# Optimization experiments

Measured on AMD Instinct MI355X. Metric: run time of the kernel, lower is better.

Reference implementation:

```python
import jax, jax.numpy as jnp
import numpy as np

INPUT_SIZE = 695 + 2 * 406 + 84  # 1591
HIDDEN = 1024
NUM_LAYERS = 2
B, T = 8, 2048


def _make_linear(key, fan_in, fan_out, forget_bias):
    kw, kb = jax.random.split(key)
    bound = 1.0 / np.sqrt(fan_in)
    W = jax.random.uniform(kw, (fan_in, fan_out), minval=-bound, maxval=bound, dtype=jnp.float32)
    b = jax.random.uniform(kb, (fan_out,), minval=-bound, maxval=bound, dtype=jnp.float32)
    H = fan_out // 3
    b = b.at[H:2 * H].set(forget_bias)  # init_input_passthrough: forget-gate bias = 6.0
    return W, b


def setup_inputs() -> dict:
    key = jax.random.key(0)
    k1, k2, k3, k4, k5 = jax.random.split(key, 5)
    prev_actions = jax.random.uniform(k1, (B, T, 695), dtype=jnp.float32)
    states = jax.random.uniform(k2, (B, T, 812), dtype=jnp.float32)
    metadata = jax.random.uniform(k3, (B, T, 84), dtype=jnp.float32)
    W1, b1 = _make_linear(k4, INPUT_SIZE, 3 * HIDDEN, 6.0)
    W2, b2 = _make_linear(k5, HIDDEN, 3 * HIDDEN, 6.0)
    return {"prev_actions": prev_actions, "states": states, "metadata": metadata,
            "W1": W1, "b1": b1, "W2": W2, "b2": b2}


def forget_mult(f, z):
    # c_t = f_t * z_t + (1 - f_t) * c_{t-1}, c_0 = 0; parallel (log-depth) scan over time.
    a = 1.0 - f          # decay
    b = f * z            # input term
    def combine(c1, c2):
        a1, b1 = c1
        a2, b2 = c2
        return a1 * a2, a2 * b1 + b2
    _, c = jax.lax.associative_scan(combine, (a, b), axis=-2)
    return c


def qrnn_layer(x, W, b):
    y = jnp.einsum('btd,dh->bth', x, W) + b          # [B,T,3H]
    Z, Fg, O = jnp.split(y, 3, axis=-1)
    C = forget_mult(jax.nn.sigmoid(Fg), jax.nn.relu(Z))  # [B,T,H]
    out = jax.nn.sigmoid(O) * C
    return out, C[..., -1, :]


def reference(prev_actions, states, metadata, W1, b1, W2, b2):
    x = jnp.concatenate([prev_actions, states, metadata], axis=-1)  # [B,T,1591]
    hs = []
    for W, b in ((W1, b1), (W2, b2)):
        x, h_last = qrnn_layer(x, W, b)
        hs.append(h_last)
    h = jnp.stack(hs, axis=-2)  # [B, num_layers, H]
    return x, h
```

## Files before the change

### kernel.cpp

```cpp
#include <hip/hip_runtime.h>

typedef unsigned short u16;
typedef unsigned int   u32;
typedef __attribute__((ext_vector_type(8))) short bf16x8;
typedef __attribute__((ext_vector_type(4))) float f32x4;
typedef __attribute__((ext_vector_type(2))) unsigned int u32x2;

#define B_ 8
#define T_ 2048
#define M_ 16384
#define N_ 3072
#define H_ 1024
#define L_ 64
#define NC_ 32

__device__ __forceinline__ u16 f2bf(float f) {
    union { float f; unsigned u; } v; v.f = f;
    unsigned r = v.u + 0x7FFFu + ((v.u >> 16) & 1u);
    return (u16)(r >> 16);
}
__device__ __forceinline__ float bf2f(u16 s) {
    union { unsigned u; float f; } v; v.u = ((unsigned)s) << 16;
    return v.f;
}
__device__ __forceinline__ float sigm(float x) {
    return 1.f / (1.f + __expf(-x));
}

__device__ __forceinline__ void gload_lds16(const void* g, void* l) {
    __builtin_amdgcn_global_load_lds(
        (const __attribute__((address_space(1))) unsigned int*)g,
        (__attribute__((address_space(3))) unsigned int*)l,
        16, 0, 0);
}

__global__ void concat_cast(const float* __restrict__ pa, const float* __restrict__ st,
                            const float* __restrict__ md, u16* __restrict__ x) {
    const int m = blockIdx.x;
    const float* pam = pa + (size_t)m * 695;
    const float* stm = st + (size_t)m * 812;
    const float* mdm = md + (size_t)m * 84;
    u16* xm = x + (size_t)m * 1600;
    for (int d = threadIdx.x; d < 1600; d += 256) {
        float v;
        if (d < 695)       v = pam[d];
        else if (d < 1507) v = stm[d - 695];
        else if (d < 1591) v = mdm[d - 1507];
        else               v = 0.f;
        xm[d] = f2bf(v);
    }
}

__global__ void wtrans(const float* __restrict__ W, u16* __restrict__ Wt, int K, int Kp) {
    __shared__ float tile[32][33];
    const int n0 = blockIdx.x << 5;
    const int k0 = blockIdx.y << 5;
    const int tx = threadIdx.x & 31, ty = threadIdx.x >> 5;
    #pragma unroll
    for (int i = 0; i < 32; i += 8) {
        int k = k0 + ty + i;
        tile[ty + i][tx] = (k < K) ? W[(size_t)k * N_ + n0 + tx] : 0.f;
    }
    __syncthreads();
    #pragma unroll
    for (int i = 0; i < 32; i += 8) {
        int n = n0 + ty + i;
        Wt[(size_t)n * Kp + k0 + tx] = f2bf(tile[tx][ty + i]);
    }
}

__global__ __launch_bounds__(512, 1)
void gemm8p(const u16* __restrict__ A, const u16* __restrict__ Bt,
            const float* __restrict__ bias, u16* __restrict__ Y,
            int Kp, int NK, int NBN) {
    __shared__ u16 lds[65536];
    const int tid = threadIdx.x;
    const int w = tid >> 6, l = tid & 63;
    const int wm = w >> 2, wn = w & 3;

    const int cpx = gridDim.x >> 3;
    const int xg = (blockIdx.x & 7) * cpx + (blockIdx.x >> 3);
    const int bm = xg / NBN, bn = xg % NBN;
    const int brow = bm << 8, bcol = bn << 8;

    const int srow = (w << 5) + (l >> 2);
    const int gslot = (l & 3) ^ ((l >> 3) & 3);
    const u16* ga = A  + (size_t)(brow + srow) * Kp + gslot * 8;
    const u16* gb = Bt + (size_t)(bcol + srow) * Kp + gslot * 8;
    const int ldst = w << 10;

    const int fl = ((l & 15) << 5) + ((((l >> 4) ^ ((l >> 1) & 3)) & 3) << 3);
    const int abase = wm << 12;
    const int bbase = 8192 + (wn << 11);

#define STG_A(r, kt) do {                                                      \
    gload_lds16(ga + (size_t)(kt) * 32,                   &lds[((r) << 14) + ldst]);        \
    gload_lds16(ga + (size_t)(kt) * 32 + 16 * (size_t)Kp, &lds[((r) << 14) + ldst + 512]);  \
} while (0)
#define STG_B(r, kt) do {                                                      \
    gload_lds16(gb + (size_t)(kt) * 32,                   &lds[((r) << 14) + 8192 + ldst]);       \
    gload_lds16(gb + (size_t)(kt) * 32 + 16 * (size_t)Kp, &lds[((r) << 14) + 8192 + ldst + 512]); \
} while (0)

    f32x4 acc[8][4] = {};
    bf16x8 bfr[4];

    STG_A(0, 0); STG_B(0, 0);
    STG_A(1, 1); STG_B(1, 1);
    STG_A(2, 2); STG_B(2, 2);
    asm volatile("s_waitcnt vmcnt(8)" ::: "memory");
    __builtin_amdgcn_s_barrier();
    asm volatile("" ::: "memory");

#define PH(CIH, LOADB, STAGECODE, WAITCODE) do {                               \
    bf16x8 af[4];                                                              \
    const int cb = cur << 14;                                                  \
    _Pragma("unroll")                                                          \
    for (int mi = 0; mi < 4; ++mi)                                             \
        af[mi] = *reinterpret_cast<const bf16x8*>(                             \
            &lds[cb + abase + (((CIH) * 4 + mi) << 9) + fl]);                  \
    if (LOADB) {                                                               \
        _Pragma("unroll")                                                      \
        for (int ni = 0; ni < 4; ++ni)                                         \
            bfr[ni] = *reinterpret_cast<const bf16x8*>(                        \
                &lds[cb + bbase + (ni << 9) + fl]);                            \
    }                                                                          \
    STAGECODE;                                                                 \
    WAITCODE;                                                                  \
    __builtin_amdgcn_s_barrier();                                              \
    __builtin_amdgcn_sched_barrier(0);                                         \
    __builtin_amdgcn_s_setprio(1);                                             \
    _Pragma("unroll")                                                          \
    for (int mi = 0; mi < 4; ++mi)                                             \
        _Pragma("unroll")                                                      \
        for (int ni = 0; ni < 4; ++ni)                                         \
            acc[(CIH) * 4 + mi][ni] = __builtin_amdgcn_mfma_f32_16x16x32_bf16( \
                bfr[ni], af[mi], acc[(CIH) * 4 + mi][ni], 0, 0, 0);            \
    __builtin_amdgcn_s_setprio(0);                                             \
    __builtin_amdgcn_sched_barrier(0);                                         \
} while (0)

    for (int kt = 0; kt < NK; ++kt) {
        const int cur = kt & 3;
        const int nxt = (kt + 3 < NK) ? kt + 3 : kt;
        const int nb = (kt + 3) & 3;
        PH(0, 1, { STG_A(nb, nxt); },
                 { asm volatile("s_waitcnt lgkmcnt(0)" ::: "memory"); });
        PH(1, 0, { STG_B(nb, nxt); },
                 { asm volatile("s_waitcnt vmcnt(8) lgkmcnt(0)" ::: "memory"); });
    }

    asm volatile("s_waitcnt vmcnt(0)" ::: "memory");
    __builtin_amdgcn_s_barrier();

    const int nloc0 = (wn << 6) + ((l >> 4) << 2);
    float4 bv4[4];
    #pragma unroll
    for (int nf = 0; nf < 4; ++nf)
        bv4[nf] = *reinterpret_cast<const float4*>(&bias[bcol + nloc0 + nf * 16]);
    #pragma unroll
    for (int ci = 0; ci < 8; ++ci) {
        const int mrow = (wm << 7) + ((ci >> 2) << 6) + ((ci & 3) << 4) + (l & 15);
        #pragma unroll
        for (int nf = 0; nf < 4; ++nf) {
            const int nloc = nloc0 + nf * 16;
            u32x2 p;
            p.x = (u32)f2bf(acc[ci][nf][0] + bv4[nf].x) |
                  ((u32)f2bf(acc[ci][nf][1] + bv4[nf].y) << 16);
            p.y = (u32)f2bf(acc[ci][nf][2] + bv4[nf].z) |
                  ((u32)f2bf(acc[ci][nf][3] + bv4[nf].w) << 16);
            const int off = (mrow << 8) + (((nloc >> 3) ^ (mrow & 7)) << 3) +
                            ((nloc >> 2) & 1) * 4;
            *reinterpret_cast<u32x2*>(&lds[off]) = p;
        }
    }
    asm volatile("s_waitcnt lgkmcnt(0)" ::: "memory");
    __builtin_amdgcn_s_barrier();

    #pragma unroll
    for (int rp = 0; rp < 16; ++rp) {
        const int row = (w << 5) + (rp << 1) + (l >> 5);
        const int c16 = l & 31;
        const bf16x8 v = *reinterpret_cast<const bf16x8*>(
            &lds[(row << 8) + ((c16 ^ (row & 7)) << 3)]);
        *reinterpret_cast<bf16x8*>(&Y[(size_t)(brow + row) * N_ + bcol + c16 * 8]) = v;
    }
#undef PH
#undef STG_A
#undef STG_B
}

__global__ void scan_p1(const u16* __restrict__ y, float* __restrict__ aprod,
                        float* __restrict__ cend) {
    const int hb = blockIdx.x & 1;
    const int chunk = (blockIdx.x >> 1) & (NC_ - 1);
    const int b = blockIdx.x >> 6;
    const int h = (hb << 9) + (threadIdx.x << 1);
    const u16* yb = y + ((size_t)b * T_ + (size_t)chunk * L_) * N_;
    float a0 = 1.f, a1 = 1.f, c0 = 0.f, c1 = 0.f;
    #pragma unroll 4
    for (int t = 0; t < L_; ++t) {
        const u32 zz = *reinterpret_cast<const u32*>(&yb[t * N_ + h]);
        const u32 ff = *reinterpret_cast<const u32*>(&yb[t * N_ + H_ + h]);
        const float f0 = sigm(bf2f((u16)ff));
        const float f1 = sigm(bf2f((u16)(ff >> 16)));
        const float z0 = fmaxf(bf2f((u16)zz), 0.f);
        const float z1 = fmaxf(bf2f((u16)(zz >> 16)), 0.f);
        c0 = f0 * z0 + (1.f - f0) * c0;  a0 *= (1.f - f0);
        c1 = f1 * z1 + (1.f - f1) * c1;  a1 *= (1.f - f1);
    }
    const size_t idx = ((size_t)b * NC_ + chunk) * H_ + h;
    *reinterpret_cast<float2*>(&aprod[idx]) = make_float2(a0, a1);
    *reinterpret_cast<float2*>(&cend[idx])  = make_float2(c0, c1);
}

__global__ void scan_p2(const float* __restrict__ aprod, const float* __restrict__ cend,
                        float* __restrict__ cin, float* __restrict__ hout, int layer) {
    const int b = blockIdx.x >> 2;
    const int h = ((blockIdx.x & 3) << 8) + threadIdx.x;
    float c = 0.f;
    #pragma unroll
    for (int k = 0; k < NC_; ++k) {
        const size_t idx = ((size_t)b * NC_ + k) * H_ + h;
        cin[idx] = c;
        c = aprod[idx] * c + cend[idx];
    }
    hout[(size_t)(((b << 1) + layer) << 10) + h] = c;
}

__global__ void scan_p3(const u16* __restrict__ y, const float* __restrict__ cin,
                        void* __restrict__ xout, int layer) {
    const int hb = blockIdx.x & 1;
    const int chunk = (blockIdx.x >> 1) & (NC_ - 1);
    const int b = blockIdx.x >> 6;
    const int h = (hb << 9) + (threadIdx.x << 1);
    const u16* yb = y + ((size_t)b * T_ + (size_t)chunk * L_) * N_;
    const size_t cidx = ((size_t)b * NC_ + chunk) * H_ + h;
    const float2 cv = *reinterpret_cast<const float2*>(&cin[cidx]);
    float c0 = cv.x, c1 = cv.y;
    u32*    xo_bf = (u32*)xout;
    float2* xo_f  = (float2*)xout;
    const size_t obase = ((size_t)b * T_ + (size_t)chunk * L_) * H_ + h;
    #pragma unroll 4
    for (int t = 0; t < L_; ++t) {
        const u32 zz = *reinterpret_cast<const u32*>(&yb[t * N_ + h]);
        const u32 ff = *reinterpret_cast<const u32*>(&yb[t * N_ + H_ + h]);
        const u32 oo = *reinterpret_cast<const u32*>(&yb[t * N_ + 2 * H_ + h]);
        const float f0 = sigm(bf2f((u16)ff));
        const float f1 = sigm(bf2f((u16)(ff >> 16)));
        const float z0 = fmaxf(bf2f((u16)zz), 0.f);
        const float z1 = fmaxf(bf2f((u16)(zz >> 16)), 0.f);
        c0 = f0 * z0 + (1.f - f0) * c0;
        c1 = f1 * z1 + (1.f - f1) * c1;
        const float o0 = sigm(bf2f((u16)oo)) * c0;
        const float o1 = sigm(bf2f((u16)(oo >> 16))) * c1;
        const size_t oi = obase + (size_t)t * H_;
        if (layer) xo_f[oi >> 1] = make_float2(o0, o1);
        else       xo_bf[oi >> 1] = (u32)f2bf(o0) | ((u32)f2bf(o1) << 16);
    }
}

extern "C" void kernel_launch(void* const* d_in, const int* in_sizes, int n_in,
                              void* d_out, int out_size, void* d_ws, size_t ws_size,
                              hipStream_t stream) {
    const float* pa = (const float*)d_in[0];
    const float* st = (const float*)d_in[1];
    const float* md = (const float*)d_in[2];
    const float* W1 = (const float*)d_in[3];
    const float* b1 = (const float*)d_in[4];
    const float* W2 = (const float*)d_in[5];
    const float* b2 = (const float*)d_in[6];
    float* out = (float*)d_out;

    char* ws = (char*)d_ws;
    const size_t y_bytes = (size_t)M_ * N_ * 2;
    const size_t x_bytes = (size_t)M_ * 1600 * 2;
    u16* y  = (u16*)ws;
    u16* x  = (u16*)(ws + y_bytes);
    u16* Wt = (u16*)(ws + y_bytes + x_bytes);
    char* scr = ws + y_bytes + (size_t)M_ * H_ * 2;
    const size_t sarr = (size_t)B_ * NC_ * H_ * 4;
    float* aprod = (float*)scr;
    float* cend  = (float*)(scr + sarr);
    float* cin   = (float*)(scr + 2 * sarr);

    float* hout = out + (size_t)M_ * H_;

    const int grid_g = (M_ / 256) * (N_ / 256);

    concat_cast<<<M_, 256, 0, stream>>>(pa, st, md, x);
    wtrans<<<dim3(N_ / 32, 50), 256, 0, stream>>>(W1, Wt, 1591, 1600);
    gemm8p<<<grid_g, 512, 0, stream>>>(x, Wt, b1, y, 1600, 50, N_ / 256);
    scan_p1<<<B_ * NC_ * 2, 256, 0, stream>>>(y, aprod, cend);
    scan_p2<<<32, 256, 0, stream>>>(aprod, cend, cin, hout, 0);
    scan_p3<<<B_ * NC_ * 2, 256, 0, stream>>>(y, cin, x, 0);

    wtrans<<<dim3(N_ / 32, 32), 256, 0, stream>>>(W2, Wt, 1024, 1024);
    gemm8p<<<grid_g, 512, 0, stream>>>(x, Wt, b2, y, 1024, 32, N_ / 256);
    scan_p1<<<B_ * NC_ * 2, 256, 0, stream>>>(y, aprod, cend);
    scan_p2<<<32, 256, 0, stream>>>(aprod, cend, cin, hout, 1);
    scan_p3<<<B_ * NC_ * 2, 256, 0, stream>>>(y, cin, out, 1);
}
```

Baseline: 431.7 us.

## Restructure GEMM main loop to K=64 double-buffered tiles with quadrant phases

The bf16 GEMM main loop changes from a 4-deep ring of K=32 tiles to two 64 KB buffers holding K=64 tiles. Each K step is split into four phases over output quadrants, and each phase stages one half-tile of A or B for the next step. Wave-to-fragment mapping and the LDS swizzle change to 8-slot XOR rows, and the epilogue index math is updated to match. Each barrier now covers more MFMA work, but prefetch depth drops to one tile, an extra barrier is added per phase, and the K-iteration count is halved at the call sites.

```diff
diff --git a/kernel.cpp b/kernel.cpp
--- a/kernel.cpp
+++ b/kernel.cpp
@@ -83,92 +83,111 @@
     const int bm = xg / NBN, bn = xg % NBN;
     const int brow = bm << 8, bcol = bn << 8;
 
-    const int srow = (w << 5) + (l >> 2);
-    const int gslot = (l & 3) ^ ((l >> 3) & 3);
-    const u16* ga = A  + (size_t)(brow + srow) * Kp + gslot * 8;
-    const u16* gb = Bt + (size_t)(bcol + srow) * Kp + gslot * 8;
-    const int ldst = w << 10;
-
-    const int fl = ((l & 15) << 5) + ((((l >> 4) ^ ((l >> 1) & 3)) & 3) << 3);
-    const int abase = wm << 12;
-    const int bbase = 8192 + (wn << 11);
-
-#define STG_A(r, kt) do {                                                      \
-    gload_lds16(ga + (size_t)(kt) * 32,                   &lds[((r) << 14) + ldst]);        \
-    gload_lds16(ga + (size_t)(kt) * 32 + 16 * (size_t)Kp, &lds[((r) << 14) + ldst + 512]);  \
+    const int gslot8 = (((l & 7) ^ ((l >> 3) & 7)) & 7) << 3;
+    const int srow = (w << 3) + (l >> 3);
+    const u16* pA = A  + (size_t)(brow + srow) * Kp + gslot8;
+    const u16* pB = Bt + (size_t)(bcol + srow) * Kp + gslot8;
+    const int wst = w << 9;
+
+    const int kslot0 = ((((l >> 4) ^ l) & 7) << 3);
+    const int aoff_l = ((wm << 4) + (l & 15)) * 64 + kslot0;
+    const int boff_l = ((wn << 4) + (l & 15)) * 64 + kslot0;
+
+#define STG_A(d, h, kt) do {                                                        \
+    gload_lds16(pA + (size_t)((h) * 128) * Kp + (size_t)(kt) * 64,                  \
+                &lds[(d) * 32768 + (h) * 8192 + wst]);                              \
+    gload_lds16(pA + (size_t)((h) * 128 + 64) * Kp + (size_t)(kt) * 64,             \
+                &lds[(d) * 32768 + (h) * 8192 + wst + 4096]);                       \
 } while (0)
-#define STG_B(r, kt) do {                                                      \
-    gload_lds16(gb + (size_t)(kt) * 32,                   &lds[((r) << 14) + 8192 + ldst]);       \
-    gload_lds16(gb + (size_t)(kt) * 32 + 16 * (size_t)Kp, &lds[((r) << 14) + 8192 + ldst + 512]); \
+#define STG_B(d, h, kt) do {                                                        \
+    gload_lds16(pB + (size_t)((h) * 128) * Kp + (size_t)(kt) * 64,                  \
+                &lds[(d) * 32768 + 16384 + (h) * 8192 + wst]);                      \
+    gload_lds16(pB + (size_t)((h) * 128 + 64) * Kp + (size_t)(kt) * 64,             \
+                &lds[(d) * 32768 + 16384 + (h) * 8192 + wst + 4096]);               \
 } while (0)
 
     f32x4 acc[8][4] = {};
-    bf16x8 bfr[4];
-
-    STG_A(0, 0); STG_B(0, 0);
-    STG_A(1, 1); STG_B(1, 1);
-    STG_A(2, 2); STG_B(2, 2);
-    asm volatile("s_waitcnt vmcnt(8)" ::: "memory");
+    bf16x8 afr[4][2], bfr[4][2];
+
+    STG_A(0, 0, 0); STG_B(0, 0, 0); STG_B(0, 1, 0); STG_A(0, 1, 0);
+    asm volatile("s_waitcnt vmcnt(4)" ::: "memory");
     __builtin_amdgcn_s_barrier();
     asm volatile("" ::: "memory");
 
-#define PH(CIH, LOADB, STAGECODE, WAITCODE) do {                               \
-    bf16x8 af[4];                                                              \
-    const int cb = cur << 14;                                                  \
-    _Pragma("unroll")                                                          \
-    for (int mi = 0; mi < 4; ++mi)                                             \
-        af[mi] = *reinterpret_cast<const bf16x8*>(                             \
-            &lds[cb + abase + (((CIH) * 4 + mi) << 9) + fl]);                  \
-    if (LOADB) {                                                               \
+#define PH(MH, NH, RDA, RDB, STAGECODE, LGK8) do {                             \
+    const int cb = cur << 15;                                                  \
+    if (RDA) {                                                                 \
+        const int ab = cb + (MH) * 8192 + aoff_l;                              \
         _Pragma("unroll")                                                      \
-        for (int ni = 0; ni < 4; ++ni)                                         \
-            bfr[ni] = *reinterpret_cast<const bf16x8*>(                        \
-                &lds[cb + bbase + (ni << 9) + fl]);                            \
+        for (int j = 0; j < 4; ++j) {                                          \
+            afr[j][0] = *reinterpret_cast<const bf16x8*>(&lds[ab + j * 2048]); \
+            afr[j][1] = *reinterpret_cast<const bf16x8*>(                      \
+                &lds[(ab + j * 2048) ^ 32]);                                   \
+        }                                                                      \
+    }                                                                          \
+    if (RDB) {                                                                 \
+        const int bb = cb + 16384 + (NH) * 8192 + boff_l;                      \
+        _Pragma("unroll")                                                      \
+        for (int j = 0; j < 2; ++j) {                                          \
+            bfr[(NH) * 2 + j][0] = *reinterpret_cast<const bf16x8*>(           \
+                &lds[bb + j * 4096]);                                          \
+            bfr[(NH) * 2 + j][1] = *reinterpret_cast<const bf16x8*>(           \
+                &lds[(bb + j * 4096) ^ 32]);                                   \
+        }                                                                      \
     }                                                                          \
     STAGECODE;                                                                 \
-    WAITCODE;                                                                  \
+    if (LGK8) asm volatile("s_waitcnt lgkmcnt(8)" ::: "memory");               \
+    asm volatile("s_waitcnt vmcnt(4)" ::: "memory");                           \
     __builtin_amdgcn_s_barrier();                                              \
+    asm volatile("s_waitcnt lgkmcnt(0)" ::: "memory");                         \
     __builtin_amdgcn_sched_barrier(0);                                         \
     __builtin_amdgcn_s_setprio(1);                                             \
     _Pragma("unroll")                                                          \
-    for (int mi = 0; mi < 4; ++mi)                                             \
+    for (int j = 0; j < 4; ++j)                                                \
         _Pragma("unroll")                                                      \
-        for (int ni = 0; ni < 4; ++ni)                                         \
-            acc[(CIH) * 4 + mi][ni] = __builtin_amdgcn_mfma_f32_16x16x32_bf16( \
-                bfr[ni], af[mi], acc[(CIH) * 4 + mi][ni], 0, 0, 0);            \
+        for (int j2 = 0; j2 < 2; ++j2)                                         \
+            _Pragma("unroll")                                                  \
+            for (int kk = 0; kk < 2; ++kk)                                     \
+                acc[(MH) * 4 + j][(NH) * 2 + j2] =                             \
+                    __builtin_amdgcn_mfma_f32_16x16x32_bf16(                   \
+                        bfr[(NH) * 2 + j2][kk], afr[j][kk],                    \
+                        acc[(MH) * 4 + j][(NH) * 2 + j2], 0, 0, 0);            \
     __builtin_amdgcn_s_setprio(0);                                             \
     __builtin_amdgcn_sched_barrier(0);                                         \
+    __builtin_amdgcn_s_barrier();                                              \
+    asm volatile("" ::: "memory");                                             \
 } while (0)
 
     for (int kt = 0; kt < NK; ++kt) {
-        const int cur = kt & 3;
-        const int nxt = (kt + 3 < NK) ? kt + 3 : kt;
-        const int nb = (kt + 3) & 3;
-        PH(0, 1, { STG_A(nb, nxt); },
-                 { asm volatile("s_waitcnt lgkmcnt(0)" ::: "memory"); });
-        PH(1, 0, { STG_B(nb, nxt); },
-                 { asm volatile("s_waitcnt vmcnt(8) lgkmcnt(0)" ::: "memory"); });
+        const int cur = kt & 1;
+        const int nb = cur ^ 1;
+        const int nxt = (kt + 1 < NK) ? kt + 1 : kt;
+        PH(0, 0, 1, 1, { STG_A(nb, 0, nxt); }, 1);
+        PH(0, 1, 0, 1, { STG_B(nb, 0, nxt); }, 0);
+        PH(1, 1, 1, 0, { STG_B(nb, 1, nxt); }, 0);
+        PH(1, 0, 0, 0, { STG_A(nb, 1, nxt); }, 0);
     }
 
     asm volatile("s_waitcnt vmcnt(0)" ::: "memory");
     __builtin_amdgcn_s_barrier();
 
-    const int nloc0 = (wn << 6) + ((l >> 4) << 2);
+    const int nq = (l >> 4) << 2;
     float4 bv4[4];
     #pragma unroll
     for (int nf = 0; nf < 4; ++nf)
-        bv4[nf] = *reinterpret_cast<const float4*>(&bias[bcol + nloc0 + nf * 16]);
-    #pragma unroll
-    for (int ci = 0; ci < 8; ++ci) {
-        const int mrow = (wm << 7) + ((ci >> 2) << 6) + ((ci & 3) << 4) + (l & 15);
+        bv4[nf] = *reinterpret_cast<const float4*>(
+            &bias[bcol + nf * 64 + (wn << 4) + nq]);
+    #pragma unroll
+    for (int mf = 0; mf < 8; ++mf) {
+        const int mrow = mf * 32 + (wm << 4) + (l & 15);
         #pragma unroll
         for (int nf = 0; nf < 4; ++nf) {
-            const int nloc = nloc0 + nf * 16;
+            const int nloc = nf * 64 + (wn << 4) + nq;
             u32x2 p;
-            p.x = (u32)f2bf(acc[ci][nf][0] + bv4[nf].x) |
-                  ((u32)f2bf(acc[ci][nf][1] + bv4[nf].y) << 16);
-            p.y = (u32)f2bf(acc[ci][nf][2] + bv4[nf].z) |
-                  ((u32)f2bf(acc[ci][nf][3] + bv4[nf].w) << 16);
+            p.x = (u32)f2bf(acc[mf][nf][0] + bv4[nf].x) |
+                  ((u32)f2bf(acc[mf][nf][1] + bv4[nf].y) << 16);
+            p.y = (u32)f2bf(acc[mf][nf][2] + bv4[nf].z) |
+                  ((u32)f2bf(acc[mf][nf][3] + bv4[nf].w) << 16);
             const int off = (mrow << 8) + (((nloc >> 3) ^ (mrow & 7)) << 3) +
                             ((nloc >> 2) & 1) * 4;
             *reinterpret_cast<u32x2*>(&lds[off]) = p;
@@ -290,13 +309,13 @@
 
     concat_cast<<<M_, 256, 0, stream>>>(pa, st, md, x);
     wtrans<<<dim3(N_ / 32, 50), 256, 0, stream>>>(W1, Wt, 1591, 1600);
-    gemm8p<<<grid_g, 512, 0, stream>>>(x, Wt, b1, y, 1600, 50, N_ / 256);
+    gemm8p<<<grid_g, 512, 0, stream>>>(x, Wt, b1, y, 1600, 25, N_ / 256);
     scan_p1<<<B_ * NC_ * 2, 256, 0, stream>>>(y, aprod, cend);
     scan_p2<<<32, 256, 0, stream>>>(aprod, cend, cin, hout, 0);
     scan_p3<<<B_ * NC_ * 2, 256, 0, stream>>>(y, cin, x, 0);
 
     wtrans<<<dim3(N_ / 32, 32), 256, 0, stream>>>(W2, Wt, 1024, 1024);
-    gemm8p<<<grid_g, 512, 0, stream>>>(x, Wt, b2, y, 1024, 32, N_ / 256);
+    gemm8p<<<grid_g, 512, 0, stream>>>(x, Wt, b2, y, 1024, 16, N_ / 256);
     scan_p1<<<B_ * NC_ * 2, 256, 0, stream>>>(y, aprod, cend);
     scan_p2<<<32, 256, 0, stream>>>(aprod, cend, cin, hout, 1);
     scan_p3<<<B_ * NC_ * 2, 256, 0, stream>>>(y, cin, out, 1);
```

After: 424.1 us. Within noise of the previous version (-1.8%).
